# Optimization experiments

Hardware: AMD Instinct MI355X
Metric: run time of the kernel (lower is better)

Reference implementation:

```python
import jax, jax.numpy as jnp
import numpy as np

N = 4_000_000

def setup_inputs() -> dict:
    key = jax.random.key(0)
    k1, k2, k3, k4 = jax.random.split(key, 4)
    return {
        "rot_kf": jax.random.normal(k1, (N, 3, 3), dtype=jnp.float32),
        "pose_kf": jax.random.normal(k2, (N, 3), dtype=jnp.float32),
        "rot_gt": jax.random.normal(k3, (N, 3, 3), dtype=jnp.float32),
        "pose_gt": jax.random.normal(k4, (N, 3), dtype=jnp.float32),
    }


def reference(rot_kf, pose_kf, rot_gt, pose_gt):
    # Per frame i: M_kf_inv @ M_gt where M_kf_inv = [R_kf^T, -R_kf^T p_kf; 0 1]
    # => relative rotation R_rel = R_kf^T @ R_gt
    #    relative translation t_rel = R_kf^T @ (p_gt - p_kf)
    # ||relative_se3 - I4||_F^2 = ||R_rel - I3||_F^2 + ||t_rel||^2
    # (bottom row [0,0,0,1] matches identity exactly)
    R_rel = jnp.einsum('nji,njk->nik', rot_kf, rot_gt)          # [N,3,3]
    t_rel = jnp.einsum('nji,nj->ni', rot_kf, pose_gt - pose_kf)  # [N,3]
    eye3 = jnp.eye(3, dtype=R_rel.dtype)
    s_error = jnp.sum((R_rel - eye3) ** 2, axis=(1, 2)) + jnp.sum(t_rel ** 2, axis=1)  # [N]
    return jnp.sqrt(jnp.mean(s_error)) + 1e-8
```

## Files before the change

### kernel.cpp

```cpp
#include <hip/hip_runtime.h>
#include <math.h>

#define BLOCK 256
#define FPT   4
#define FPC   (BLOCK * FPT)
#define NBLOCKS 2048

#define ROT_F4_PER_CHUNK (FPC * 9 / 4)

__global__ __launch_bounds__(BLOCK) void rmse_partial_kernel(
    const float* __restrict__ rot_kf, const float* __restrict__ pose_kf,
    const float* __restrict__ rot_gt, const float* __restrict__ pose_gt,
    float* __restrict__ partial, int N)
{
    __shared__ float lds[FPC * 9];
    __shared__ float redbuf[BLOCK / 64];

    const int tid = threadIdx.x;
    const long long totalRot = (long long)N * 9;
    const int nChunks = (N + FPC - 1) / FPC;

    float sum = 0.0f;
    float a[FPT][9];

    for (int c = blockIdx.x; c < nChunks; c += gridDim.x) {
        const long long base4 = (long long)c * ROT_F4_PER_CHUNK;

        __syncthreads();
        #pragma unroll
        for (int j = 0; j < 9; ++j) {
            const long long f4 = base4 + (long long)j * BLOCK + tid;
            const long long e  = f4 * 4;
            float4 v;
            if (e + 3 < totalRot) {
                v = reinterpret_cast<const float4*>(rot_kf)[f4];
            } else {
                v.x = (e + 0 < totalRot) ? rot_kf[e + 0] : 0.0f;
                v.y = (e + 1 < totalRot) ? rot_kf[e + 1] : 0.0f;
                v.z = (e + 2 < totalRot) ? rot_kf[e + 2] : 0.0f;
                v.w = 0.0f;
            }
            reinterpret_cast<float4*>(lds)[j * BLOCK + tid] = v;
        }
        __syncthreads();
        #pragma unroll
        for (int s = 0; s < FPT; ++s) {
            #pragma unroll
            for (int j = 0; j < 9; ++j) a[s][j] = lds[(s * BLOCK + tid) * 9 + j];
        }
        __syncthreads();

        #pragma unroll
        for (int j = 0; j < 9; ++j) {
            const long long f4 = base4 + (long long)j * BLOCK + tid;
            const long long e  = f4 * 4;
            float4 v;
            if (e + 3 < totalRot) {
                v = reinterpret_cast<const float4*>(rot_gt)[f4];
            } else {
                v.x = (e + 0 < totalRot) ? rot_gt[e + 0] : 0.0f;
                v.y = (e + 1 < totalRot) ? rot_gt[e + 1] : 0.0f;
                v.z = (e + 2 < totalRot) ? rot_gt[e + 2] : 0.0f;
                v.w = 0.0f;
            }
            reinterpret_cast<float4*>(lds)[j * BLOCK + tid] = v;
        }
        __syncthreads();

        #pragma unroll
        for (int s = 0; s < FPT; ++s) {
            const int frame = c * FPC + s * BLOCK + tid;
            if (frame < N) {
                float b[9];
                #pragma unroll
                for (int j = 0; j < 9; ++j) b[j] = lds[(s * BLOCK + tid) * 9 + j];

                const long long p = (long long)frame * 3;
                const float d0 = pose_gt[p + 0] - pose_kf[p + 0];
                const float d1 = pose_gt[p + 1] - pose_kf[p + 1];
                const float d2 = pose_gt[p + 2] - pose_kf[p + 2];

                float s_err = 0.0f;
                #pragma unroll
                for (int i = 0; i < 3; ++i) {
                    #pragma unroll
                    for (int k = 0; k < 3; ++k) {
                        float r = a[s][i] * b[k] + a[s][3 + i] * b[3 + k] + a[s][6 + i] * b[6 + k];
                        r -= (i == k) ? 1.0f : 0.0f;
                        s_err += r * r;
                    }
                    const float t = a[s][i] * d0 + a[s][3 + i] * d1 + a[s][6 + i] * d2;
                    s_err += t * t;
                }
                sum += s_err;
            }
        }
    }

    const int lane = tid & 63;
    const int wave = tid >> 6;
    #pragma unroll
    for (int off = 32; off > 0; off >>= 1) sum += __shfl_down(sum, off);
    if (lane == 0) redbuf[wave] = sum;
    __syncthreads();
    if (tid == 0) {
        float s = 0.0f;
        #pragma unroll
        for (int w = 0; w < BLOCK / 64; ++w) s += redbuf[w];
        partial[blockIdx.x] = s;
    }
}

__global__ __launch_bounds__(BLOCK) void rmse_finalize_kernel(
    const float* __restrict__ partial, int nPartial, float* __restrict__ out, int N)
{
    __shared__ float redbuf[BLOCK / 64];
    float sum = 0.0f;
    for (int i = threadIdx.x; i < nPartial; i += BLOCK) sum += partial[i];
    #pragma unroll
    for (int off = 32; off > 0; off >>= 1) sum += __shfl_down(sum, off);
    const int lane = threadIdx.x & 63;
    const int wave = threadIdx.x >> 6;
    if (lane == 0) redbuf[wave] = sum;
    __syncthreads();
    if (threadIdx.x == 0) {
        float s = 0.0f;
        #pragma unroll
        for (int w = 0; w < BLOCK / 64; ++w) s += redbuf[w];
        out[0] = sqrtf(s / (float)N) + 1e-8f;
    }
}

extern "C" void kernel_launch(void* const* d_in, const int* in_sizes, int n_in,
                              void* d_out, int out_size, void* d_ws, size_t ws_size,
                              hipStream_t stream) {
    const float* rot_kf  = (const float*)d_in[0];
    const float* pose_kf = (const float*)d_in[1];
    const float* rot_gt  = (const float*)d_in[2];
    const float* pose_gt = (const float*)d_in[3];
    float* out = (float*)d_out;
    float* partial = (float*)d_ws;

    const int N = in_sizes[1] / 3;
    const int nChunks = (N + FPC - 1) / FPC;

    int grid = NBLOCKS;
    if (grid > nChunks) grid = nChunks;
    const int wsCap = (int)(ws_size / sizeof(float));
    if (grid > wsCap) grid = wsCap;
    if (grid < 1) grid = 1;

    rmse_partial_kernel<<<grid, BLOCK, 0, stream>>>(rot_kf, pose_kf, rot_gt, pose_gt, partial, N);
    rmse_finalize_kernel<<<1, BLOCK, 0, stream>>>(partial, grid, out, N);
}
```

Baseline: 72.62 us.

## Double-buffer rotation loads via global_load_lds with manual waitcnt pipelining

After: 74.90 us. +3.1%, slower.

```diff
diff --git a/kernel.cpp b/kernel.cpp
--- a/kernel.cpp
+++ b/kernel.cpp
@@ -3,69 +3,71 @@
 
 #define BLOCK 256
 #define FPT   4
-#define FPC   (BLOCK * FPT)
-#define NBLOCKS 2048
+#define FPC   1024
+#define F4_PER_STAGE 2304
+#define MAXBLOCKS 2048
 
-#define ROT_F4_PER_CHUNK (FPC * 9 / 4)
+#define GLOAD_LDS16(gp, lp)                                                     \
+  __builtin_amdgcn_global_load_lds(                                             \
+      (const __attribute__((address_space(1))) void*)(gp),                      \
+      (__attribute__((address_space(3))) void*)(lp), 16, 0, 0)
 
-__global__ __launch_bounds__(BLOCK) void rmse_partial_kernel(
+__global__ __launch_bounds__(BLOCK, 2) void rmse_partial_kernel(
     const float* __restrict__ rot_kf, const float* __restrict__ pose_kf,
     const float* __restrict__ rot_gt, const float* __restrict__ pose_gt,
     float* __restrict__ partial, int N)
 {
-    __shared__ float lds[FPC * 9];
+    __shared__ float lds[2][FPC * 9];
     __shared__ float redbuf[BLOCK / 64];
 
     const int tid = threadIdx.x;
-    const long long totalRot = (long long)N * 9;
-    const int nChunks = (N + FPC - 1) / FPC;
+    const long long totalRotF = (long long)N * 9;
+    const long long f4max = (totalRotF >= 4) ? (totalRotF - 4) / 4 : 0;
+    const int nChunks = (int)(((long long)N + FPC - 1) / FPC);
+    const int stride = gridDim.x;
 
     float sum = 0.0f;
-    float a[FPT][9];
 
-    for (int c = blockIdx.x; c < nChunks; c += gridDim.x) {
-        const long long base4 = (long long)c * ROT_F4_PER_CHUNK;
-
-        __syncthreads();
+    auto issue = [&](const float* __restrict__ src, float* ldsBuf, int cc) {
+        const long long base4 = (long long)cc * F4_PER_STAGE;
         #pragma unroll
         for (int j = 0; j < 9; ++j) {
-            const long long f4 = base4 + (long long)j * BLOCK + tid;
-            const long long e  = f4 * 4;
-            float4 v;
-            if (e + 3 < totalRot) {
-                v = reinterpret_cast<const float4*>(rot_kf)[f4];
-            } else {
-                v.x = (e + 0 < totalRot) ? rot_kf[e + 0] : 0.0f;
-                v.y = (e + 1 < totalRot) ? rot_kf[e + 1] : 0.0f;
-                v.z = (e + 2 < totalRot) ? rot_kf[e + 2] : 0.0f;
-                v.w = 0.0f;
-            }
-            reinterpret_cast<float4*>(lds)[j * BLOCK + tid] = v;
+            long long f4 = base4 + j * BLOCK + tid;
+            if (f4 > f4max) f4 = f4max;
+            GLOAD_LDS16(reinterpret_cast<const float4*>(src) + f4,
+                        ldsBuf + (size_t)(j * BLOCK + tid) * 4);
         }
-        __syncthreads();
+    };
+
+    int c = blockIdx.x;
+    if (c < nChunks) {
+        issue(rot_kf, lds[0], c);
+        issue(rot_gt, lds[1], c);
+    }
+
+    while (c < nChunks) {
+        const int cn = c + stride;
+        const bool hasNext = (cn < nChunks);
+
+        asm volatile("s_waitcnt vmcnt(9)" ::: "memory");
+        __builtin_amdgcn_sched_barrier(0);
+        __builtin_amdgcn_s_barrier();
+
+        float a[FPT][9];
         #pragma unroll
         for (int s = 0; s < FPT; ++s) {
             #pragma unroll
-            for (int j = 0; j < 9; ++j) a[s][j] = lds[(s * BLOCK + tid) * 9 + j];
+            for (int j = 0; j < 9; ++j) a[s][j] = lds[0][(s * BLOCK + tid) * 9 + j];
         }
-        __syncthreads();
+        asm volatile("s_waitcnt lgkmcnt(0)" ::: "memory");
+        __builtin_amdgcn_sched_barrier(0);
+        __builtin_amdgcn_s_barrier();
+        if (hasNext) issue(rot_kf, lds[0], cn);
 
-        #pragma unroll
-        for (int j = 0; j < 9; ++j) {
-            const long long f4 = base4 + (long long)j * BLOCK + tid;
-            const long long e  = f4 * 4;
-            float4 v;
-            if (e + 3 < totalRot) {
-                v = reinterpret_cast<const float4*>(rot_gt)[f4];
-            } else {
-                v.x = (e + 0 < totalRot) ? rot_gt[e + 0] : 0.0f;
-                v.y = (e + 1 < totalRot) ? rot_gt[e + 1] : 0.0f;
-                v.z = (e + 2 < totalRot) ? rot_gt[e + 2] : 0.0f;
-                v.w = 0.0f;
-            }
-            reinterpret_cast<float4*>(lds)[j * BLOCK + tid] = v;
-        }
-        __syncthreads();
+        if (hasNext) { asm volatile("s_waitcnt vmcnt(9)" ::: "memory"); }
+        else         { asm volatile("s_waitcnt vmcnt(0)" ::: "memory"); }
+        __builtin_amdgcn_sched_barrier(0);
+        __builtin_amdgcn_s_barrier();
 
         #pragma unroll
         for (int s = 0; s < FPT; ++s) {
@@ -73,28 +75,34 @@
             if (frame < N) {
                 float b[9];
                 #pragma unroll
-                for (int j = 0; j < 9; ++j) b[j] = lds[(s * BLOCK + tid) * 9 + j];
+                for (int j = 0; j < 9; ++j) b[j] = lds[1][(s * BLOCK + tid) * 9 + j];
 
                 const long long p = (long long)frame * 3;
                 const float d0 = pose_gt[p + 0] - pose_kf[p + 0];
                 const float d1 = pose_gt[p + 1] - pose_kf[p + 1];
                 const float d2 = pose_gt[p + 2] - pose_kf[p + 2];
 
-                float s_err = 0.0f;
+                float se = 0.0f;
                 #pragma unroll
                 for (int i = 0; i < 3; ++i) {
                     #pragma unroll
                     for (int k = 0; k < 3; ++k) {
                         float r = a[s][i] * b[k] + a[s][3 + i] * b[3 + k] + a[s][6 + i] * b[6 + k];
                         r -= (i == k) ? 1.0f : 0.0f;
-                        s_err += r * r;
+                        se += r * r;
                     }
                     const float t = a[s][i] * d0 + a[s][3 + i] * d1 + a[s][6 + i] * d2;
-                    s_err += t * t;
+                    se += t * t;
                 }
-                sum += s_err;
+                sum += se;
             }
         }
+        asm volatile("s_waitcnt lgkmcnt(0)" ::: "memory");
+        __builtin_amdgcn_sched_barrier(0);
+        __builtin_amdgcn_s_barrier();
+        if (hasNext) issue(rot_gt, lds[1], cn);
+
+        c = cn;
     }
 
     const int lane = tid & 63;
@@ -142,10 +150,10 @@
     float* partial = (float*)d_ws;
 
     const int N = in_sizes[1] / 3;
-    const int nChunks = (N + FPC - 1) / FPC;
+    const int nChunks = (int)(((long long)N + FPC - 1) / FPC);
 
-    int grid = NBLOCKS;
-    if (grid > nChunks) grid = nChunks;
+    int grid = (nChunks + 1) / 2;
+    if (grid > MAXBLOCKS) grid = MAXBLOCKS;
     const int wsCap = (int)(ws_size / sizeof(float));
     if (grid > wsCap) grid = wsCap;
     if (grid < 1) grid = 1;
```
